# Kernel tuning notes

Hardware: AMD Instinct MI355X
Metric: run time of the kernel (lower is better)

## Reference

```python
import jax, jax.numpy as jnp
import numpy as np

NUM_HEADS = 16  # init_kwargs num_heads


def setup_inputs() -> dict:
    key = jax.random.key(0)
    ks = jax.random.split(key, 3)
    B, S, D = 4, 2048, 1024
    scale = 1.0 / np.sqrt(D)
    return {
        "x": jax.random.normal(ks[0], (B, S, D), dtype=jnp.float32),
        "in_proj_w": jax.random.normal(ks[1], (3 * D, D), dtype=jnp.float32) * scale,
        "in_proj_b": jnp.zeros((3 * D,), dtype=jnp.float32),
        "out_w": jax.random.normal(ks[2], (D, D), dtype=jnp.float32) * scale,
        "out_b": jnp.zeros((D,), dtype=jnp.float32),
        "gamma": jnp.ones((D,), dtype=jnp.float32),
        "beta": jnp.zeros((D,), dtype=jnp.float32),
    }


def reference(x, in_proj_w, in_proj_b, out_w, out_b, gamma, beta):
    B, S, D = x.shape
    H = NUM_HEADS
    hd = D // H
    # packed qkv projection (torch Linear convention: y = x @ W.T + b)
    qkv = x @ in_proj_w.T + in_proj_b            # [B,S,3D]
    q, k, v = jnp.split(qkv, 3, axis=-1)
    q = q.reshape(B, S, H, hd).transpose(0, 2, 1, 3)  # [B,H,S,hd]
    k = k.reshape(B, S, H, hd).transpose(0, 2, 1, 3)
    v = v.reshape(B, S, H, hd).transpose(0, 2, 1, 3)

    scores = jnp.einsum("bhqd,bhkd->bhqk", q, k) / jnp.sqrt(jnp.asarray(hd, x.dtype))
    # additive causal mask: -inf above the diagonal
    causal = jnp.tril(jnp.ones((S, S), dtype=bool))
    scores = jnp.where(causal, scores, jnp.asarray(-jnp.inf, scores.dtype))
    attn = jax.nn.softmax(scores, axis=-1)       # [B,H,S,S]

    ctx = jnp.einsum("bhqk,bhkd->bhqd", attn, v)  # [B,H,S,hd]
    ctx = ctx.transpose(0, 2, 1, 3).reshape(B, S, D)
    attn_out = ctx @ out_w.T + out_b

    y = x + attn_out
    mu = jnp.mean(y, axis=-1, keepdims=True)
    var = jnp.mean(jnp.square(y - mu), axis=-1, keepdims=True)
    y = (y - mu) * jax.lax.rsqrt(var + 1e-5) * gamma + beta
    return y
```

## Files before the change

### kernel.cpp

```cpp
#include <hip/hip_runtime.h>
#include <stdint.h>

typedef unsigned short u16;
typedef __bf16 bf16x8 __attribute__((ext_vector_type(8)));
typedef float  f32x4  __attribute__((ext_vector_type(4)));
typedef int    i32x4  __attribute__((ext_vector_type(4)));

__device__ __forceinline__ u16 f2bf(float f){
  union{float f; uint32_t u;} v; v.f = f;
  uint32_t r = v.u + 0x7FFFu + ((v.u >> 16) & 1u);
  return (u16)(r >> 16);
}

#define GLDS16(gp, lp) __builtin_amdgcn_global_load_lds( \
    (const __attribute__((address_space(1))) void*)(gp),  \
    (__attribute__((address_space(3))) void*)(lp), 16, 0, 0)

__global__ __launch_bounds__(256) void cvt_kernel(const float* __restrict__ in,
                                                  u16* __restrict__ out, int n4) {
  int stride = gridDim.x * blockDim.x;
  for (int i = blockIdx.x * blockDim.x + threadIdx.x; i < n4; i += stride) {
    float4 v = ((const float4*)in)[i];
    u16 o0 = f2bf(v.x), o1 = f2bf(v.y), o2 = f2bf(v.z), o3 = f2bf(v.w);
    u16* p = out + (size_t)i * 4;
    uint32_t lo = (uint32_t)o0 | ((uint32_t)o1 << 16);
    uint32_t hi = (uint32_t)o2 | ((uint32_t)o3 << 16);
    ((uint2*)p)[0] = make_uint2(lo, hi);
  }
}

template <int MODE>
__global__ __launch_bounds__(256) void gemm_bt(
    const u16* __restrict__ A, const u16* __restrict__ B,
    const float* __restrict__ bias,
    u16* __restrict__ Cbf, float* __restrict__ Cf, const float* __restrict__ resid,
    int M, int N, int K) {
  __shared__ u16 Alds[128 * 32];
  __shared__ u16 Blds[128 * 32];
  const int t = threadIdx.x;
  const int w = t >> 6, l = t & 63;
  const int wr = w >> 1, wc = w & 1;
  const int g = l >> 4, r16 = l & 15;

  const int gx = gridDim.x;
  const int nwg = gx * gridDim.y;
  const int wg = blockIdx.y * gx + blockIdx.x;
  const int cpx = nwg >> 3;
  const int swz = (wg & 7) * cpx + (wg >> 3);
  const int brow = (swz / gx) * 128, bcol = (swz % gx) * 128;

  f32x4 acc[4][4];
#pragma unroll
  for (int mi = 0; mi < 4; mi++)
#pragma unroll
    for (int nj = 0; nj < 4; nj++) acc[mi][nj] = (f32x4){0.f, 0.f, 0.f, 0.f};

  const int c0 = 2 * w, c1 = 2 * w + 1;
  const int srow0 = c0 * 16 + (l >> 2);
  const int srow1 = c1 * 16 + (l >> 2);
  const int scol = (l & 3) * 8;

  for (int kt = 0; kt < K; kt += 32) {
    __syncthreads();
    GLDS16(A + (size_t)(brow + srow0) * K + kt + scol, (char*)Alds + c0 * 1024);
    GLDS16(A + (size_t)(brow + srow1) * K + kt + scol, (char*)Alds + c1 * 1024);
    GLDS16(B + (size_t)(bcol + srow0) * K + kt + scol, (char*)Blds + c0 * 1024);
    GLDS16(B + (size_t)(bcol + srow1) * K + kt + scol, (char*)Blds + c1 * 1024);
    __syncthreads();

    bf16x8 af[4], bfr[4];
#pragma unroll
    for (int mi = 0; mi < 4; mi++)
      af[mi] = *(const bf16x8*)&Alds[(wr * 64 + mi * 16 + r16) * 32 + g * 8];
#pragma unroll
    for (int nj = 0; nj < 4; nj++)
      bfr[nj] = *(const bf16x8*)&Blds[(wc * 64 + nj * 16 + r16) * 32 + g * 8];
#pragma unroll
    for (int mi = 0; mi < 4; mi++)
#pragma unroll
      for (int nj = 0; nj < 4; nj++)
        acc[mi][nj] = __builtin_amdgcn_mfma_f32_16x16x32_bf16(af[mi], bfr[nj], acc[mi][nj], 0, 0, 0);
  }

#pragma unroll
  for (int mi = 0; mi < 4; mi++) {
#pragma unroll
    for (int nj = 0; nj < 4; nj++) {
      int col = bcol + wc * 64 + nj * 16 + r16;
      float bv = bias[col];
#pragma unroll
      for (int rr = 0; rr < 4; rr++) {
        int row = brow + wr * 64 + mi * 16 + g * 4 + rr;
        float v = acc[mi][nj][rr] + bv;
        if (MODE == 0) {
          Cbf[(size_t)row * N + col] = f2bf(v);
        } else {
          v += resid[(size_t)row * N + col];
          Cf[(size_t)row * N + col] = v;
        }
      }
    }
  }
}

__global__ __launch_bounds__(256) void vtrans_kernel(const u16* __restrict__ qkv,
                                                     u16* __restrict__ vtg) {
  const int S = 2048, HD3 = 3072;
  __shared__ u16 Vs[64 * 64];
  const int st = blockIdx.x, h = blockIdx.y, b = blockIdx.z;
  const int t = threadIdx.x;
  const int s0 = st * 64;
#pragma unroll
  for (int i = 0; i < 2; i++) {
    int n = t + i * 256;
    int row = n >> 3, c = n & 7;
    const u16* src = qkv + ((size_t)(b * S) + s0 + row) * HD3 + 2048 + h * 64 + c * 8;
    i32x4 v = *(const i32x4*)src;
    *(i32x4*)&Vs[row * 64 + ((c ^ (row & 7)) << 3)] = v;
  }
  __syncthreads();
  const int d = t >> 2;
  const int dc = d >> 3, dl = d & 7;
#pragma unroll
  for (int i = 0; i < 2; i++) {
    int kc = (t & 3) + i * 4;
    u16 tmp[8];
#pragma unroll
    for (int j = 0; j < 8; j++) {
      int k = kc * 8 + j;
      tmp[j] = Vs[k * 64 + ((dc ^ (k & 7)) << 3) + dl];
    }
    *(i32x4*)(vtg + ((size_t)(b * 16 + h) * 64 + d) * S + s0 + kc * 8) = *(i32x4*)tmp;
  }
}

__global__ __launch_bounds__(256) void attn_kernel(const u16* __restrict__ qkv,
                                                   const u16* __restrict__ vtg,
                                                   u16* __restrict__ ctxb) {
  const int S = 2048, HD3 = 3072;
  __shared__ u16 Kl[2][64 * 64];
  __shared__ u16 Vl[2][64 * 64];
  __shared__ u16 Pb[4][16 * 64];

  const int h = blockIdx.x & 15, b = blockIdx.x >> 4;
  const int pair = blockIdx.y;
  const int t = threadIdx.x, w = t >> 6, l = t & 63;
  const int g = l >> 4, r16 = l & 15;
  const size_t bS = (size_t)b * S;
  const size_t vbase = ((size_t)(b * 16 + h)) * 64 * S;

  const int srow = t >> 3, ssl = t & 7;
  const int scol = ((ssl ^ (srow & 7)) << 3);
  const int sdst = w * 1024;

  int kfo[4][2], pwo[4][2], pro[2];
#pragma unroll
  for (int f = 0; f < 4; f++) {
    int row = f * 16 + r16;
#pragma unroll
    for (int c = 0; c < 2; c++)
      kfo[f][c] = (row * 64 + (((c * 4 + g) ^ (row & 7)) << 3)) * 2;
#pragma unroll
    for (int q2 = 0; q2 < 2; q2++) {
      int kidx = f * 16 + g * 4 + q2 * 2;
      pwo[f][q2] = r16 * 128 + (((kidx >> 3) ^ (r16 & 7)) << 4) + ((kidx & 7) << 1);
    }
  }
#pragma unroll
  for (int kh = 0; kh < 2; kh++)
    pro[kh] = r16 * 128 + (((kh * 4 + g) ^ (r16 & 7)) << 4);

  const float QSC = 0.125f * 1.44269504f;
  char* PW = (char*)Pb + w * 2048;

#define STAGE(bi_)                                                            \
  do {                                                                        \
    GLDS16(kp, (char*)Kl + (bi_)*8192 + sdst);                                \
    GLDS16(kp + 32 * HD3, (char*)Kl + (bi_)*8192 + 4096 + sdst);              \
    GLDS16(vp, (char*)Vl + (bi_)*8192 + sdst);                                \
    GLDS16(vp + 32 * S, (char*)Vl + (bi_)*8192 + 4096 + sdst);                \
    kp += 64 * HD3; vp += 64;                                                 \
  } while (0)

  for (int seg = 0; seg < 2; seg++) {
    const int qi = seg ? (31 - pair) : pair;
    const int qmin = qi * 64 + w * 16;
    const int nt = qi + 1;

    const u16* qp = qkv + (bS + qmin + r16) * HD3 + h * 64 + g * 8;
    bf16x8 qf0 = *(const bf16x8*)qp;
    bf16x8 qf1 = *(const bf16x8*)(qp + 32);
#pragma unroll
    for (int j = 0; j < 8; j++) {
      qf0[j] = (__bf16)((float)qf0[j] * QSC);
      qf1[j] = (__bf16)((float)qf1[j] * QSC);
    }

    f32x4 ctx[4];
#pragma unroll
    for (int f = 0; f < 4; f++) ctx[f] = (f32x4){0.f, 0.f, 0.f, 0.f};
    float mrun = -1e30f, lrun = 0.f;

    const u16* kp = qkv + (bS + srow) * HD3 + 1024 + h * 64 + scol;
    const u16* vp = vtg + vbase + (size_t)srow * S + scol;

    __syncthreads();
    STAGE(0);
    int cur = 0;
    for (int kt = 0; kt < nt; kt++) {
      const int k0 = kt * 64;
      asm volatile("s_waitcnt vmcnt(0)" ::: "memory");
      __syncthreads();
      if (kt + 1 < nt) STAGE(cur ^ 1);

      const char* KB = (const char*)Kl + cur * 8192;
      const char* VB = (const char*)Vl + cur * 8192;

      f32x4 sf[4];
      __builtin_amdgcn_s_setprio(1);
#pragma unroll
      for (int f = 0; f < 4; f++) {
        bf16x8 k0f = *(const bf16x8*)(KB + kfo[f][0]);
        bf16x8 k1f = *(const bf16x8*)(KB + kfo[f][1]);
        f32x4 s = (f32x4){0.f, 0.f, 0.f, 0.f};
        s = __builtin_amdgcn_mfma_f32_16x16x32_bf16(k0f, qf0, s, 0, 0, 0);
        s = __builtin_amdgcn_mfma_f32_16x16x32_bf16(k1f, qf1, s, 0, 0, 0);
        sf[f] = s;
      }
      __builtin_amdgcn_s_setprio(0);

      const int qg = qmin + r16;
      if (k0 + 64 > qmin) {
#pragma unroll
        for (int f = 0; f < 4; f++)
#pragma unroll
          for (int rr = 0; rr < 4; rr++)
            if (k0 + f * 16 + g * 4 + rr > qg) sf[f][rr] = -1e30f;
      }

      float tm = sf[0][0];
#pragma unroll
      for (int f = 0; f < 4; f++)
#pragma unroll
        for (int rr = 0; rr < 4; rr++) tm = fmaxf(tm, sf[f][rr]);
      tm = fmaxf(tm, __shfl_xor(tm, 16, 64));
      tm = fmaxf(tm, __shfl_xor(tm, 32, 64));

      const float mold = mrun;
      const bool skip = __all(tm <= mold + 8.0f);
      const float mnew = skip ? mold : fmaxf(mold, tm);
      mrun = mnew;

      float p[4][4];
      float ps = 0.f;
#pragma unroll
      for (int f = 0; f < 4; f++)
#pragma unroll
        for (int rr = 0; rr < 4; rr++) {
          p[f][rr] = exp2f(sf[f][rr] - mnew);
          ps += p[f][rr];
        }
      ps += __shfl_xor(ps, 16, 64);
      ps += __shfl_xor(ps, 32, 64);

      if (skip) {
        lrun += ps;
      } else {
        float sc = exp2f(mold - mnew);
        lrun = lrun * sc + ps;
#pragma unroll
        for (int rr = 0; rr < 4; rr++) {
          float scq = __shfl(sc, g * 4 + rr, 64);
#pragma unroll
          for (int f = 0; f < 4; f++) ctx[f][rr] *= scq;
        }
      }

#pragma unroll
      for (int f = 0; f < 4; f++)
#pragma unroll
        for (int q2 = 0; q2 < 2; q2++) {
          union { __bf16 b; u16 u; } a0, a1;
          a0.b = (__bf16)p[f][q2 * 2];
          a1.b = (__bf16)p[f][q2 * 2 + 1];
          *(uint32_t*)(PW + pwo[f][q2]) = (uint32_t)a0.u | ((uint32_t)a1.u << 16);
        }

      bf16x8 pf[2];
#pragma unroll
      for (int kh = 0; kh < 2; kh++) pf[kh] = *(const bf16x8*)(PW + pro[kh]);
      __builtin_amdgcn_s_setprio(1);
#pragma unroll
      for (int f = 0; f < 4; f++)
#pragma unroll
        for (int kh = 0; kh < 2; kh++) {
          bf16x8 vf = *(const bf16x8*)(VB + kfo[f][kh]);
          ctx[f] = __builtin_amdgcn_mfma_f32_16x16x32_bf16(pf[kh], vf, ctx[f], 0, 0, 0);
        }
      __builtin_amdgcn_s_setprio(0);
      cur ^= 1;
    }

    float linv = 1.f / lrun;
#pragma unroll
    for (int rr = 0; rr < 4; rr++) {
      float li = __shfl(linv, g * 4 + rr, 64);
      int qg = qmin + g * 4 + rr;
#pragma unroll
      for (int f = 0; f < 4; f++) {
        union { __bf16 b; u16 u; } o;
        o.b = (__bf16)(ctx[f][rr] * li);
        ctxb[(bS + qg) * 1024 + h * 64 + f * 16 + r16] = o.u;
      }
    }
  }
#undef STAGE
}

__global__ __launch_bounds__(256) void ln_kernel(float* __restrict__ y,
                                                 const float* __restrict__ gamma,
                                                 const float* __restrict__ beta) {
  __shared__ float sh[4];
  const int row = blockIdx.x, t = threadIdx.x;
  const int w = t >> 6, l = t & 63;
  float4 v = ((const float4*)(y + (size_t)row * 1024))[t];
  float s = v.x + v.y + v.z + v.w;
#pragma unroll
  for (int m = 32; m; m >>= 1) s += __shfl_xor(s, m, 64);
  if (l == 0) sh[w] = s;
  __syncthreads();
  float mu = (sh[0] + sh[1] + sh[2] + sh[3]) * (1.0f / 1024.0f);
  float dx = v.x - mu, dy = v.y - mu, dz = v.z - mu, dw = v.w - mu;
  float ss = dx * dx + dy * dy + dz * dz + dw * dw;
#pragma unroll
  for (int m = 32; m; m >>= 1) ss += __shfl_xor(ss, m, 64);
  __syncthreads();
  if (l == 0) sh[w] = ss;
  __syncthreads();
  float var = (sh[0] + sh[1] + sh[2] + sh[3]) * (1.0f / 1024.0f);
  float rs = rsqrtf(var + 1e-5f);
  float4 gm = ((const float4*)gamma)[t];
  float4 bt = ((const float4*)beta)[t];
  float4 o;
  o.x = dx * rs * gm.x + bt.x;
  o.y = dy * rs * gm.y + bt.y;
  o.z = dz * rs * gm.z + bt.z;
  o.w = dw * rs * gm.w + bt.w;
  ((float4*)(y + (size_t)row * 1024))[t] = o;
}

extern "C" void kernel_launch(void* const* d_in, const int* in_sizes, int n_in,
                              void* d_out, int out_size, void* d_ws, size_t ws_size,
                              hipStream_t stream) {
  (void)in_sizes; (void)n_in; (void)out_size; (void)ws_size;
  const float* x     = (const float*)d_in[0];
  const float* w1    = (const float*)d_in[1];
  const float* b1    = (const float*)d_in[2];
  const float* w2    = (const float*)d_in[3];
  const float* b2    = (const float*)d_in[4];
  const float* gamma = (const float*)d_in[5];
  const float* beta  = (const float*)d_in[6];
  float* out = (float*)d_out;

  const int M = 8192, D = 1024, N1 = 3072;

  char* ws = (char*)d_ws;
  u16* x_bf   = (u16*)(ws);
  u16* w1_bf  = (u16*)(ws + 16777216);
  u16* w2_bf  = (u16*)(ws + 23068672);
  u16* qkv_bf = (u16*)(ws + 25165824);
  u16* ctx_bf = (u16*)(ws + 75497472);
  u16* vtg    = (u16*)(ws);

  cvt_kernel<<<2048, 256, 0, stream>>>(x, x_bf, M * D / 4);
  cvt_kernel<<<1024, 256, 0, stream>>>(w1, w1_bf, N1 * D / 4);
  cvt_kernel<<<512, 256, 0, stream>>>(w2, w2_bf, D * D / 4);

  gemm_bt<0><<<dim3(N1 / 128, M / 128), 256, 0, stream>>>(
      x_bf, w1_bf, b1, qkv_bf, nullptr, nullptr, M, N1, D);

  vtrans_kernel<<<dim3(32, 16, 4), 256, 0, stream>>>(qkv_bf, vtg);

  attn_kernel<<<dim3(64, 16), 256, 0, stream>>>(qkv_bf, vtg, ctx_bf);

  gemm_bt<1><<<dim3(D / 128, M / 128), 256, 0, stream>>>(
      ctx_bf, w2_bf, b2, nullptr, out, x, M, D, D);

  ln_kernel<<<M, 256, 0, stream>>>(out, gamma, beta);
}
```

Baseline: 307.5 us.

## Rework attention kernel around 32x32x16 MFMA with register-resident P and tile-per-block

The attention kernel switches from 16x16x32 to 32x32x16 bf16 MFMA, with each wave owning 32 query rows and each block covering a 128-row query tile. The old two-segment pairing of tiles per block is removed, so each block handles one tile. The P matrix is no longer written to and read back from LDS; it is packed with v_cvt_pk_bf16_f32 and rearranged across lanes with v_permlane32_swap. The output is staged through LDS so global stores are coalesced 16-byte writes. Dropping the pairing can worsen load balance under the causal mask, and the larger accumulators raise register pressure.

```diff
diff --git a/kernel.cpp b/kernel.cpp
--- a/kernel.cpp
+++ b/kernel.cpp
@@ -4,12 +4,19 @@
 typedef unsigned short u16;
 typedef __bf16 bf16x8 __attribute__((ext_vector_type(8)));
 typedef float  f32x4  __attribute__((ext_vector_type(4)));
+typedef float  f32x16 __attribute__((ext_vector_type(16)));
 typedef int    i32x4  __attribute__((ext_vector_type(4)));
 
 __device__ __forceinline__ u16 f2bf(float f){
   union{float f; uint32_t u;} v; v.f = f;
   uint32_t r = v.u + 0x7FFFu + ((v.u >> 16) & 1u);
   return (u16)(r >> 16);
+}
+
+__device__ __forceinline__ uint32_t cvtpk(float a, float b){
+  uint32_t r;
+  asm("v_cvt_pk_bf16_f32 %0, %1, %2" : "=v"(r) : "v"(a), "v"(b));
+  return r;
 }
 
 #define GLDS16(gp, lp) __builtin_amdgcn_global_load_lds( \
@@ -140,12 +147,11 @@
   const int S = 2048, HD3 = 3072;
   __shared__ u16 Kl[2][64 * 64];
   __shared__ u16 Vl[2][64 * 64];
-  __shared__ u16 Pb[4][16 * 64];
 
   const int h = blockIdx.x & 15, b = blockIdx.x >> 4;
-  const int pair = blockIdx.y;
+  const int qi = 15 - (int)blockIdx.y;
   const int t = threadIdx.x, w = t >> 6, l = t & 63;
-  const int g = l >> 4, r16 = l & 15;
+  const int l31 = l & 31, hi = l >> 5;
   const size_t bS = (size_t)b * S;
   const size_t vbase = ((size_t)(b * 16 + h)) * 64 * S;
 
@@ -153,25 +159,39 @@
   const int scol = ((ssl ^ (srow & 7)) << 3);
   const int sdst = w * 1024;
 
-  int kfo[4][2], pwo[4][2], pro[2];
-#pragma unroll
-  for (int f = 0; f < 4; f++) {
-    int row = f * 16 + r16;
-#pragma unroll
-    for (int c = 0; c < 2; c++)
-      kfo[f][c] = (row * 64 + (((c * 4 + g) ^ (row & 7)) << 3)) * 2;
-#pragma unroll
-    for (int q2 = 0; q2 < 2; q2++) {
-      int kidx = f * 16 + g * 4 + q2 * 2;
-      pwo[f][q2] = r16 * 128 + (((kidx >> 3) ^ (r16 & 7)) << 4) + ((kidx & 7) << 1);
+  int kro[4], vro[2][2];
+#pragma unroll
+  for (int hs = 0; hs < 4; hs++)
+    kro[hs] = l31 * 128 + (((2 * hs + hi) ^ (l31 & 7)) << 4);
+#pragma unroll
+  for (int ks = 0; ks < 2; ks++)
+#pragma unroll
+    for (int s2 = 0; s2 < 2; s2++)
+      vro[ks][s2] = l31 * 128 + (((ks * 4 + s2 * 2 + hi) ^ (l31 & 7)) << 4);
+
+  const float QSC = 0.125f * 1.44269504f;
+  const int q0w = qi * 128 + w * 32;
+  const int qv = q0w + l31;
+  const int nt = 2 * qi + 2;
+
+  bf16x8 qfr[4];
+  {
+    const u16* qp = qkv + (bS + qv) * HD3 + h * 64 + hi * 8;
+#pragma unroll
+    for (int hs = 0; hs < 4; hs++) {
+      bf16x8 a = *(const bf16x8*)(qp + hs * 16);
+#pragma unroll
+      for (int j = 0; j < 8; j++) a[j] = (__bf16)((float)a[j] * QSC);
+      qfr[hs] = a;
     }
   }
-#pragma unroll
-  for (int kh = 0; kh < 2; kh++)
-    pro[kh] = r16 * 128 + (((kh * 4 + g) ^ (r16 & 7)) << 4);
-
-  const float QSC = 0.125f * 1.44269504f;
-  char* PW = (char*)Pb + w * 2048;
+
+  f32x16 o[2];
+  o[0] = (f32x16)(0.f); o[1] = (f32x16)(0.f);
+  float mrun = -1e30f, lrun = 0.f;
+
+  const u16* kp = qkv + (bS + srow) * HD3 + 1024 + h * 64 + scol;
+  const u16* vp = vtg + vbase + (size_t)srow * S + scol;
 
 #define STAGE(bi_)                                                            \
   do {                                                                        \
@@ -182,68 +202,47 @@
     kp += 64 * HD3; vp += 64;                                                 \
   } while (0)
 
-  for (int seg = 0; seg < 2; seg++) {
-    const int qi = seg ? (31 - pair) : pair;
-    const int qmin = qi * 64 + w * 16;
-    const int nt = qi + 1;
-
-    const u16* qp = qkv + (bS + qmin + r16) * HD3 + h * 64 + g * 8;
-    bf16x8 qf0 = *(const bf16x8*)qp;
-    bf16x8 qf1 = *(const bf16x8*)(qp + 32);
-#pragma unroll
-    for (int j = 0; j < 8; j++) {
-      qf0[j] = (__bf16)((float)qf0[j] * QSC);
-      qf1[j] = (__bf16)((float)qf1[j] * QSC);
-    }
-
-    f32x4 ctx[4];
-#pragma unroll
-    for (int f = 0; f < 4; f++) ctx[f] = (f32x4){0.f, 0.f, 0.f, 0.f};
-    float mrun = -1e30f, lrun = 0.f;
-
-    const u16* kp = qkv + (bS + srow) * HD3 + 1024 + h * 64 + scol;
-    const u16* vp = vtg + vbase + (size_t)srow * S + scol;
-
+  STAGE(0);
+  int cur = 0;
+  for (int kt = 0; kt < nt; kt++) {
+    const int k0 = kt * 64;
+    asm volatile("s_waitcnt vmcnt(0)" ::: "memory");
     __syncthreads();
-    STAGE(0);
-    int cur = 0;
-    for (int kt = 0; kt < nt; kt++) {
-      const int k0 = kt * 64;
-      asm volatile("s_waitcnt vmcnt(0)" ::: "memory");
-      __syncthreads();
-      if (kt + 1 < nt) STAGE(cur ^ 1);
-
+    if (kt + 1 < nt) STAGE(cur ^ 1);
+
+    if (k0 < q0w + 32) {
       const char* KB = (const char*)Kl + cur * 8192;
       const char* VB = (const char*)Vl + cur * 8192;
 
-      f32x4 sf[4];
+      f32x16 s[2];
       __builtin_amdgcn_s_setprio(1);
 #pragma unroll
-      for (int f = 0; f < 4; f++) {
-        bf16x8 k0f = *(const bf16x8*)(KB + kfo[f][0]);
-        bf16x8 k1f = *(const bf16x8*)(KB + kfo[f][1]);
-        f32x4 s = (f32x4){0.f, 0.f, 0.f, 0.f};
-        s = __builtin_amdgcn_mfma_f32_16x16x32_bf16(k0f, qf0, s, 0, 0, 0);
-        s = __builtin_amdgcn_mfma_f32_16x16x32_bf16(k1f, qf1, s, 0, 0, 0);
-        sf[f] = s;
+      for (int ks = 0; ks < 2; ks++) {
+        f32x16 a = (f32x16)(0.f);
+#pragma unroll
+        for (int hs = 0; hs < 4; hs++) {
+          bf16x8 kf = *(const bf16x8*)(KB + ks * 4096 + kro[hs]);
+          a = __builtin_amdgcn_mfma_f32_32x32x16_bf16(kf, qfr[hs], a, 0, 0, 0);
+        }
+        s[ks] = a;
       }
       __builtin_amdgcn_s_setprio(0);
 
-      const int qg = qmin + r16;
-      if (k0 + 64 > qmin) {
-#pragma unroll
-        for (int f = 0; f < 4; f++)
-#pragma unroll
-          for (int rr = 0; rr < 4; rr++)
-            if (k0 + f * 16 + g * 4 + rr > qg) sf[f][rr] = -1e30f;
-      }
-
-      float tm = sf[0][0];
-#pragma unroll
-      for (int f = 0; f < 4; f++)
-#pragma unroll
-        for (int rr = 0; rr < 4; rr++) tm = fmaxf(tm, sf[f][rr]);
-      tm = fmaxf(tm, __shfl_xor(tm, 16, 64));
+      if (k0 + 63 > q0w) {
+#pragma unroll
+        for (int ks = 0; ks < 2; ks++)
+#pragma unroll
+          for (int r = 0; r < 16; r++) {
+            int kg = k0 + ks * 32 + ((r & 3) + 8 * (r >> 2) + 4 * hi);
+            if (kg > qv) s[ks][r] = -1e30f;
+          }
+      }
+
+      float tm = s[0][0];
+#pragma unroll
+      for (int ks = 0; ks < 2; ks++)
+#pragma unroll
+        for (int r = 0; r < 16; r++) tm = fmaxf(tm, s[ks][r]);
       tm = fmaxf(tm, __shfl_xor(tm, 32, 64));
 
       const float mold = mrun;
@@ -251,67 +250,79 @@
       const float mnew = skip ? mold : fmaxf(mold, tm);
       mrun = mnew;
 
-      float p[4][4];
       float ps = 0.f;
 #pragma unroll
-      for (int f = 0; f < 4; f++)
-#pragma unroll
-        for (int rr = 0; rr < 4; rr++) {
-          p[f][rr] = exp2f(sf[f][rr] - mnew);
-          ps += p[f][rr];
+      for (int ks = 0; ks < 2; ks++)
+#pragma unroll
+        for (int r = 0; r < 16; r++) {
+          float e = __builtin_amdgcn_exp2f(s[ks][r] - mnew);
+          s[ks][r] = e;
+          ps += e;
         }
-      ps += __shfl_xor(ps, 16, 64);
       ps += __shfl_xor(ps, 32, 64);
 
       if (skip) {
         lrun += ps;
       } else {
-        float sc = exp2f(mold - mnew);
+        float sc = __builtin_amdgcn_exp2f(mold - mnew);
         lrun = lrun * sc + ps;
 #pragma unroll
-        for (int rr = 0; rr < 4; rr++) {
-          float scq = __shfl(sc, g * 4 + rr, 64);
-#pragma unroll
-          for (int f = 0; f < 4; f++) ctx[f][rr] *= scq;
+        for (int dt = 0; dt < 2; dt++)
+#pragma unroll
+          for (int r = 0; r < 16; r++) o[dt][r] *= sc;
+      }
+
+#pragma unroll
+      for (int ks = 0; ks < 2; ks++) {
+        uint32_t wk0 = cvtpk(s[ks][0],  s[ks][1]);
+        uint32_t wk1 = cvtpk(s[ks][2],  s[ks][3]);
+        uint32_t wk2 = cvtpk(s[ks][4],  s[ks][5]);
+        uint32_t wk3 = cvtpk(s[ks][6],  s[ks][7]);
+        uint32_t wk4 = cvtpk(s[ks][8],  s[ks][9]);
+        uint32_t wk5 = cvtpk(s[ks][10], s[ks][11]);
+        uint32_t wk6 = cvtpk(s[ks][12], s[ks][13]);
+        uint32_t wk7 = cvtpk(s[ks][14], s[ks][15]);
+        asm("v_permlane32_swap_b32 %0, %1" : "+v"(wk0), "+v"(wk2));
+        asm("v_permlane32_swap_b32 %0, %1" : "+v"(wk1), "+v"(wk3));
+        asm("v_permlane32_swap_b32 %0, %1" : "+v"(wk4), "+v"(wk6));
+        asm("v_permlane32_swap_b32 %0, %1" : "+v"(wk5), "+v"(wk7));
+        union { uint32_t u[4]; bf16x8 v; } p0, p1;
+        p0.u[0] = wk0; p0.u[1] = wk1; p0.u[2] = wk2; p0.u[3] = wk3;
+        p1.u[0] = wk4; p1.u[1] = wk5; p1.u[2] = wk6; p1.u[3] = wk7;
+
+        __builtin_amdgcn_s_setprio(1);
+#pragma unroll
+        for (int dt = 0; dt < 2; dt++) {
+          bf16x8 vf0 = *(const bf16x8*)(VB + dt * 4096 + vro[ks][0]);
+          bf16x8 vf1 = *(const bf16x8*)(VB + dt * 4096 + vro[ks][1]);
+          o[dt] = __builtin_amdgcn_mfma_f32_32x32x16_bf16(vf0, p0.v, o[dt], 0, 0, 0);
+          o[dt] = __builtin_amdgcn_mfma_f32_32x32x16_bf16(vf1, p1.v, o[dt], 0, 0, 0);
         }
-      }
-
-#pragma unroll
-      for (int f = 0; f < 4; f++)
-#pragma unroll
-        for (int q2 = 0; q2 < 2; q2++) {
-          union { __bf16 b; u16 u; } a0, a1;
-          a0.b = (__bf16)p[f][q2 * 2];
-          a1.b = (__bf16)p[f][q2 * 2 + 1];
-          *(uint32_t*)(PW + pwo[f][q2]) = (uint32_t)a0.u | ((uint32_t)a1.u << 16);
-        }
-
-      bf16x8 pf[2];
-#pragma unroll
-      for (int kh = 0; kh < 2; kh++) pf[kh] = *(const bf16x8*)(PW + pro[kh]);
-      __builtin_amdgcn_s_setprio(1);
-#pragma unroll
-      for (int f = 0; f < 4; f++)
-#pragma unroll
-        for (int kh = 0; kh < 2; kh++) {
-          bf16x8 vf = *(const bf16x8*)(VB + kfo[f][kh]);
-          ctx[f] = __builtin_amdgcn_mfma_f32_16x16x32_bf16(pf[kh], vf, ctx[f], 0, 0, 0);
-        }
-      __builtin_amdgcn_s_setprio(0);
-      cur ^= 1;
+        __builtin_amdgcn_s_setprio(0);
+      }
     }
-
+    cur ^= 1;
+  }
+
+  {
     float linv = 1.f / lrun;
-#pragma unroll
-    for (int rr = 0; rr < 4; rr++) {
-      float li = __shfl(linv, g * 4 + rr, 64);
-      int qg = qmin + g * 4 + rr;
-#pragma unroll
-      for (int f = 0; f < 4; f++) {
-        union { __bf16 b; u16 u; } o;
-        o.b = (__bf16)(ctx[f][rr] * li);
-        ctxb[(bS + qg) * 1024 + h * 64 + f * 16 + r16] = o.u;
-      }
+    char* Ob = ((w < 2) ? (char*)Kl : (char*)Vl) + cur * 8192 + (w & 1) * 4096;
+#pragma unroll
+    for (int dt = 0; dt < 2; dt++)
+#pragma unroll
+      for (int i = 0; i < 8; i++) {
+        uint32_t pk = cvtpk(o[dt][2 * i] * linv, o[dt][2 * i + 1] * linv);
+        int d = dt * 32 + 8 * (i >> 1) + 2 * (i & 1) + 4 * hi;
+        int c8 = d >> 3;
+        *(uint32_t*)(Ob + l31 * 128 + ((c8 ^ (l31 & 7)) << 4) + ((d & 7) << 1)) = pk;
+      }
+    asm volatile("s_waitcnt lgkmcnt(0)" ::: "memory");
+#pragma unroll
+    for (int bq = 0; bq < 4; bq++) {
+      int qr = bq * 8 + (l >> 3);
+      int c = l & 7;
+      i32x4 vvv = *(const i32x4*)(Ob + qr * 128 + ((c ^ (qr & 7)) << 4));
+      *(i32x4*)(ctxb + (bS + q0w + qr) * 1024 + h * 64 + c * 8) = vvv;
     }
   }
 #undef STAGE
```

After: 283.5 us. 1.08x faster.
